# Kernel optimization log

Measured on AMD Instinct MI355X. Metric: run time of the kernel, lower is better.

Reference implementation:

```python
import jax, jax.numpy as jnp
import numpy as np

B, S, D, H = 2, 2048, 1024, 16
HD = D // H  # head dim = 64

def setup_inputs() -> dict:
    key = jax.random.key(0)
    k1, k2, k3, k4, k5 = jax.random.split(key, 5)
    return {
        "x": jax.random.normal(k1, (B, S, D), dtype=jnp.float32),
        "w_qkv": jax.random.normal(k2, (D, 3 * D), dtype=jnp.float32) * (1.0 / np.sqrt(D)),
        "b_qkv": jax.random.normal(k3, (3 * D,), dtype=jnp.float32) * 0.02,
        "w_out": jax.random.normal(k4, (D, D), dtype=jnp.float32) * (1.0 / np.sqrt(D)),
        "b_out": jax.random.normal(k5, (D,), dtype=jnp.float32) * 0.02,
        "c": 0,
    }

def reference(x, w_qkv, b_qkv, w_out, b_out, c):
    # fused QKV projection: [B,S,3D]
    qkv = jnp.einsum('bsd,de->bse', x, w_qkv) + b_qkv
    q, k, v = jnp.split(qkv, 3, axis=-1)
    # [B,S,D] -> [B,H,S,HD]
    split_heads = lambda t: t.reshape(B, S, H, HD).transpose(0, 2, 1, 3)
    q, k, v = split_heads(q), split_heads(k), split_heads(v)
    scale = 1.0 / np.sqrt(HD).astype(np.float32)
    scores = jnp.einsum('bhqd,bhkd->bhqk', q, k) * scale  # [B,H,S,S]
    probs = jax.nn.softmax(scores, axis=-1)
    # c==1 noise path references an undefined `const` in the original (dead/broken);
    # dropout probs are 0 -> identity (eval mode).
    attn = jnp.einsum('bhqk,bhkd->bhqd', probs, v)  # [B,H,S,HD]
    attn = attn.transpose(0, 2, 1, 3).reshape(B, S, D)
    out = jnp.einsum('bsd,de->bse', attn, w_out) + b_out
    return out
```

## Files before the change

### kernel.cpp

```cpp
#include <hip/hip_runtime.h>


typedef __attribute__((ext_vector_type(8))) short bs8;
typedef __attribute__((ext_vector_type(4))) short bs4;
typedef __attribute__((ext_vector_type(4))) float f32x4;

__device__ __forceinline__ f32x4 MFMA16K16(bs4 a, bs4 b, f32x4 c) {
#if defined(__HIP_DEVICE_COMPILE__)
  return __builtin_amdgcn_mfma_f32_16x16x16bf16_1k(a, b, c, 0, 0, 0);
#else
  return c;
#endif
}

#define QSCALE 0.18033688011112042f
#define MBOUND 24.0f

__device__ __forceinline__ unsigned short f2bf(float f) {
  union { float f; unsigned int u; } v; v.f = f;
  return (unsigned short)((v.u + 0x8000u) >> 16);
}

__device__ __forceinline__ unsigned int pkbf2(float a, float b) {
  union { float f; unsigned int u; } va, vb; va.f = a; vb.f = b;
#if defined(__HIP_DEVICE_COMPILE__)
  return __builtin_amdgcn_perm(vb.u + 0x8000u, va.u + 0x8000u, 0x07060302u);
#else
  return 0u;
#endif
}

__device__ __forceinline__ void async16(const unsigned short* g, unsigned short* lds) {
  __builtin_amdgcn_global_load_lds(
      (const __attribute__((address_space(1))) unsigned int*)g,
      (__attribute__((address_space(3))) unsigned int*)lds, 16, 0, 0);
}

__device__ __forceinline__ void stage_rows64(unsigned short* lds, const unsigned short* src,
                                             int ldk, int w, int l) {
#pragma unroll
  for (int i = 0; i < 4; ++i) {
    int row = (w * 4 + i) * 8 + (l >> 3);
    int cg  = (l & 7) ^ (l >> 3);
    async16(src + (size_t)row * ldk + cg * 8, lds + (w * 4 + i) * 512);
  }
}

__device__ __forceinline__ void stage_vt(unsigned short* lds, const unsigned short* vtb,
                                         int keyofs, int w, int l) {
#pragma unroll
  for (int i = 0; i < 4; ++i) {
    int row = (w * 4 + i) * 4 + (l >> 4);
    int cg = (l & 15) ^ (row & 15);
    async16(vtb + (size_t)row * 2048 + keyofs + cg * 8, lds + (w * 4 + i) * 512);
  }
}

__global__ __launch_bounds__(256) void cast_bf16_kernel(const float* __restrict__ src,
                                                        unsigned short* __restrict__ dst, int n) {
  int i = (blockIdx.x * 256 + threadIdx.x) * 8;
  if (i >= n) return;
  float4 a = *(const float4*)(src + i);
  float4 b = *(const float4*)(src + i + 4);
  union { bs8 v; unsigned short u[8]; } o;
  o.u[0] = f2bf(a.x); o.u[1] = f2bf(a.y); o.u[2] = f2bf(a.z); o.u[3] = f2bf(a.w);
  o.u[4] = f2bf(b.x); o.u[5] = f2bf(b.y); o.u[6] = f2bf(b.z); o.u[7] = f2bf(b.w);
  *(bs8*)(dst + i) = o.v;
}

__global__ __launch_bounds__(256) void transpose_cast_kernel(const float* __restrict__ src,
                                                             unsigned short* __restrict__ dst,
                                                             int R, int C) {
  __shared__ unsigned short tile[64][73];
  int c0 = blockIdx.x * 64, r0 = blockIdx.y * 64;
  int t = threadIdx.x;
  int rl = t >> 2, cb = (t & 3) * 16;
  const float* p = src + (size_t)(r0 + rl) * C + c0 + cb;
#pragma unroll
  for (int j = 0; j < 16; j += 4) {
    float4 f = *(const float4*)(p + j);
    tile[rl][cb + j + 0] = f2bf(f.x);
    tile[rl][cb + j + 1] = f2bf(f.y);
    tile[rl][cb + j + 2] = f2bf(f.z);
    tile[rl][cb + j + 3] = f2bf(f.w);
  }
  __syncthreads();
  int cl = t >> 2, rb = (t & 3) * 16;
  unsigned short* q = dst + (size_t)(c0 + cl) * R + r0 + rb;
#pragma unroll
  for (int j = 0; j < 16; ++j) q[j] = tile[rb + j][cl];
}

__global__ __launch_bounds__(256) void transpose_v_kernel(const unsigned short* __restrict__ v,
                                                          unsigned short* __restrict__ vt) {
  __shared__ unsigned short tile[64][73];
  int s0 = blockIdx.x * 64, bh = blockIdx.y;
  int t = threadIdx.x;
  int sl = t >> 2, hb = (t & 3) * 16;
  const unsigned short* p = v + ((size_t)bh * 2048 + s0 + sl) * 64 + hb;
#pragma unroll
  for (int j = 0; j < 16; ++j) tile[sl][hb + j] = p[j];
  __syncthreads();
  int hl = t >> 2, sb = (t & 3) * 16;
  unsigned short* q = vt + ((size_t)bh * 64 + hl) * 2048 + s0 + sb;
#pragma unroll
  for (int j = 0; j < 16; ++j) q[j] = tile[sb + j][hl];
}

#define GEMM_CORE(A_, Bt_)                                                        \
  __shared__ unsigned short As[128 * 64];                                         \
  __shared__ unsigned short Bs[128 * 64];                                         \
  int t = threadIdx.x, w = t >> 6, l = t & 63;                                    \
  int wm = w >> 1, wn = w & 1;                                                    \
  int bm = blockIdx.y, bn = blockIdx.x;                                           \
  const unsigned short* Abase = (A_) + (size_t)bm * 128 * 1024;                   \
  const unsigned short* Bbase = (Bt_) + (size_t)bn * 128 * 1024;                  \
  f32x4 zero4 = {0.f, 0.f, 0.f, 0.f};                                             \
  f32x4 acc[4][4];                                                                \
  _Pragma("unroll") for (int i = 0; i < 4; ++i)                                   \
  _Pragma("unroll") for (int j = 0; j < 4; ++j) acc[i][j] = zero4;                \
  for (int kt = 0; kt < 16; ++kt) {                                               \
    stage_rows64(As, Abase + kt * 64, 1024, w, l);                                \
    stage_rows64(Bs, Bbase + kt * 64, 1024, w, l);                                \
    __syncthreads();                                                              \
    _Pragma("unroll") for (int ks = 0; ks < 2; ++ks) {                            \
      bs8 af[4], bf[4];                                                           \
      _Pragma("unroll") for (int mt = 0; mt < 4; ++mt) {                          \
        int row = wm * 64 + mt * 16 + (l & 15);                                   \
        int c = ks * 4 + (l >> 4);                                                \
        af[mt] = *(const bs8*)&As[row * 64 + ((c ^ (row & 7)) * 8)];              \
      }                                                                           \
      _Pragma("unroll") for (int nt = 0; nt < 4; ++nt) {                          \
        int row = wn * 64 + nt * 16 + (l & 15);                                   \
        int c = ks * 4 + (l >> 4);                                                \
        bf[nt] = *(const bs8*)&Bs[row * 64 + ((c ^ (row & 7)) * 8)];              \
      }                                                                           \
      _Pragma("unroll") for (int mt = 0; mt < 4; ++mt)                            \
      _Pragma("unroll") for (int nt = 0; nt < 4; ++nt)                            \
        acc[mt][nt] = __builtin_amdgcn_mfma_f32_16x16x32_bf16(af[mt], bf[nt],     \
                                                              acc[mt][nt], 0, 0, 0); \
    }                                                                             \
    __syncthreads();                                                              \
  }

__global__ __launch_bounds__(256) void gemm_qkv_kernel(const unsigned short* __restrict__ A,
                                                       const unsigned short* __restrict__ Bt,
                                                       const float* __restrict__ bias,
                                                       unsigned short* __restrict__ qo,
                                                       unsigned short* __restrict__ ko,
                                                       unsigned short* __restrict__ vo) {
  GEMM_CORE(A, Bt)
#pragma unroll
  for (int nt = 0; nt < 4; ++nt) {
    int ng = bn * 128 + wn * 64 + nt * 16 + (l & 15);
    float bb = bias[ng];
    int sect = ng >> 10;
    int f = ng & 1023, h = f >> 6, hd = f & 63;
    unsigned short* dst = (sect == 0) ? qo : (sect == 1) ? ko : vo;
    float sc = (sect == 0) ? QSCALE : 1.0f;
#pragma unroll
    for (int mt = 0; mt < 4; ++mt)
#pragma unroll
      for (int r = 0; r < 4; ++r) {
        int mg = bm * 128 + wm * 64 + mt * 16 + (l >> 4) * 4 + r;
        int b = mg >> 11, s = mg & 2047;
        float val = (acc[mt][nt][r] + bb) * sc;
        dst[((size_t)(b * 16 + h) * 2048 + s) * 64 + hd] = f2bf(val);
      }
  }
}

__global__ __launch_bounds__(256) void gemm_out_kernel(const unsigned short* __restrict__ A,
                                                       const unsigned short* __restrict__ Bt,
                                                       const float* __restrict__ bias,
                                                       float* __restrict__ out) {
  GEMM_CORE(A, Bt)
#pragma unroll
  for (int nt = 0; nt < 4; ++nt) {
    int ng = bn * 128 + wn * 64 + nt * 16 + (l & 15);
    float bb = bias[ng];
#pragma unroll
    for (int mt = 0; mt < 4; ++mt)
#pragma unroll
      for (int r = 0; r < 4; ++r) {
        int mg = bm * 128 + wm * 64 + mt * 16 + (l >> 4) * 4 + r;
        out[(size_t)mg * 1024 + ng] = acc[mt][nt][r] + bb;
      }
  }
}

__global__ __launch_bounds__(256, 2) void attn_kernel(const unsigned short* __restrict__ Q,
                                                      const unsigned short* __restrict__ K,
                                                      const unsigned short* __restrict__ Vt,
                                                      unsigned short* __restrict__ Aout) {
  __shared__ unsigned short Ks[2][128 * 64];
  __shared__ unsigned short Vts[2][64 * 128];
  int t = threadIdx.x, w = t >> 6, l = t & 63;
  int m16 = l & 15, q = l >> 4;
  int qt = blockIdx.x, bh = blockIdx.y;
  const unsigned short* qbase = Q + (size_t)bh * 2048 * 64 + (size_t)qt * 128 * 64;
  const unsigned short* kbase = K + (size_t)bh * 2048 * 64;
  const unsigned short* vtbase = Vt + (size_t)bh * 64 * 2048;

  bs8 qf[2][2];
#pragma unroll
  for (int mt = 0; mt < 2; ++mt)
#pragma unroll
    for (int ks = 0; ks < 2; ++ks)
      qf[mt][ks] = *(const bs8*)(qbase + (size_t)(w * 32 + mt * 16 + m16) * 64 + ks * 32 + q * 8);

  stage_rows64(&Ks[0][0], kbase, 64, w, l);
  stage_vt(&Vts[0][0], vtbase, 0, w, l);
  __syncthreads();

  f32x4 zero4 = {0.f, 0.f, 0.f, 0.f};
  f32x4 minit = {-MBOUND, -MBOUND, -MBOUND, -MBOUND};
  f32x4 o[2][4];
  float lst[2] = {0.f, 0.f};
#pragma unroll
  for (int mt = 0; mt < 2; ++mt)
#pragma unroll
    for (int nh = 0; nh < 4; ++nh) o[mt][nh] = zero4;

  for (int kt = 0; kt < 16; ++kt) {
    int buf = kt & 1;
    if (kt < 15) {
      stage_rows64(&Ks[buf ^ 1][0], kbase + (size_t)(kt + 1) * 128 * 64, 64, w, l);
      stage_vt(&Vts[buf ^ 1][0], vtbase, (kt + 1) * 128, w, l);
    }
    const unsigned short* Kb = &Ks[buf][0];
    const unsigned short* Vb = &Vts[buf][0];

    f32x4 sAcc[2][8];
#pragma unroll
    for (int mt = 0; mt < 2; ++mt)
#pragma unroll
      for (int nt = 0; nt < 8; ++nt) sAcc[mt][nt] = minit;
#pragma unroll
    for (int ks = 0; ks < 2; ++ks) {
      bs8 kf[8];
#pragma unroll
      for (int nt = 0; nt < 8; ++nt) {
        int row = nt * 16 + m16;
        int c = ks * 4 + q;
        kf[nt] = *(const bs8*)&Kb[row * 64 + ((c ^ (row & 7)) * 8)];
      }
#pragma unroll
      for (int nt = 0; nt < 8; ++nt)
#pragma unroll
        for (int mt = 0; mt < 2; ++mt)
          sAcc[mt][nt] = __builtin_amdgcn_mfma_f32_16x16x32_bf16(kf[nt], qf[mt][ks],
                                                                 sAcc[mt][nt], 0, 0, 0);
    }

#pragma unroll
    for (int mt = 0; mt < 2; ++mt) {
      float rs = 0.f;
#pragma unroll
      for (int nt = 0; nt < 8; ++nt)
#pragma unroll
        for (int r = 0; r < 4; ++r) {
          float p = __builtin_amdgcn_exp2f(sAcc[mt][nt][r]);
          sAcc[mt][nt][r] = p;
          rs += p;
        }
      lst[mt] += rs;
    }

#pragma unroll
    for (int nt = 0; nt < 8; ++nt) {
      bs4 vf[4];
#pragma unroll
      for (int nh = 0; nh < 4; ++nh) {
        int vrow = nh * 16 + m16;
        int k = nt * 16 + q * 4;
        int chunk = k >> 3, within = k & 7;
        vf[nh] = *(const bs4*)&Vb[vrow * 128 + ((chunk ^ (vrow & 15)) * 8) + within];
      }
#pragma unroll
      for (int mt = 0; mt < 2; ++mt) {
        union { bs4 v; unsigned int u[2]; } pf;
        pf.u[0] = pkbf2(sAcc[mt][nt][0], sAcc[mt][nt][1]);
        pf.u[1] = pkbf2(sAcc[mt][nt][2], sAcc[mt][nt][3]);
#pragma unroll
        for (int nh = 0; nh < 4; ++nh)
          o[mt][nh] = MFMA16K16(vf[nh], pf.v, o[mt][nh]);
      }
    }
    __syncthreads();
  }

  int b = bh >> 4, h = bh & 15;
#pragma unroll
  for (int mt = 0; mt < 2; ++mt) {
    float l0 = lst[mt];
    l0 += __shfl_xor(l0, 16);
    l0 += __shfl_xor(l0, 32);
    float inv = 1.0f / l0;
    int s = qt * 128 + w * 32 + mt * 16 + m16;
#pragma unroll
    for (int nh = 0; nh < 4; ++nh)
#pragma unroll
      for (int r = 0; r < 4; ++r) {
        int hd = nh * 16 + q * 4 + r;
        Aout[((size_t)(b * 2048 + s)) * 1024 + h * 64 + hd] = f2bf(o[mt][nh][r] * inv);
      }
  }
}

extern "C" void kernel_launch(void* const* d_in, const int* in_sizes, int n_in,
                              void* d_out, int out_size, void* d_ws, size_t ws_size,
                              hipStream_t stream) {
  const float* x     = (const float*)d_in[0];
  const float* w_qkv = (const float*)d_in[1];
  const float* b_qkv = (const float*)d_in[2];
  const float* w_out = (const float*)d_in[3];
  const float* b_out = (const float*)d_in[4];
  float* out = (float*)d_out;

  char* ws = (char*)d_ws;
  unsigned short* xb    = (unsigned short*)(ws);
  unsigned short* wt1   = (unsigned short*)(ws + (8u << 20));
  unsigned short* wt2   = (unsigned short*)(ws + (14u << 20));
  unsigned short* qb    = (unsigned short*)(ws + (16u << 20));
  unsigned short* kb    = (unsigned short*)(ws + (24u << 20));
  unsigned short* vb    = (unsigned short*)(ws + (32u << 20));
  unsigned short* vtb   = (unsigned short*)(ws + (40u << 20));
  unsigned short* attnb = (unsigned short*)(ws + (48u << 20));

  cast_bf16_kernel<<<2048, 256, 0, stream>>>(x, xb, 4194304);
  transpose_cast_kernel<<<dim3(48, 16), 256, 0, stream>>>(w_qkv, wt1, 1024, 3072);
  transpose_cast_kernel<<<dim3(16, 16), 256, 0, stream>>>(w_out, wt2, 1024, 1024);
  gemm_qkv_kernel<<<dim3(24, 32), 256, 0, stream>>>(xb, wt1, b_qkv, qb, kb, vb);
  transpose_v_kernel<<<dim3(32, 32), 256, 0, stream>>>(vb, vtb);
  attn_kernel<<<dim3(16, 32), 256, 0, stream>>>(qb, kb, vtb, attnb);
  gemm_out_kernel<<<dim3(8, 32), 256, 0, stream>>>(attnb, wt2, b_out, out);
}
```

Before: 209.0 us.

## Swizzle V-transpose layout to cut LDS bank conflicts; use 8 waves in out-projection GEMM

The V transpose kernel now writes each row with a 4-element swap inside 8-element groups for half of the head-dim rows. The attention kernel's V fragment reads apply the matching inverse swizzle, which is meant to reduce LDS bank conflicts on the bs4 reads. Separately, the output-projection GEMM runs 512 threads (8 waves) per 128x128 tile, each wave holding a 32x64 sub-tile, to raise occupancy and latency hiding. The cost is more barrier participants and a smaller MFMA tile per wave, and the V layout now depends on a cross-kernel swizzle contract that must stay consistent.

```diff
diff --git a/kernel.cpp b/kernel.cpp
--- a/kernel.cpp
+++ b/kernel.cpp
@@ -43,6 +43,16 @@
     int row = (w * 4 + i) * 8 + (l >> 3);
     int cg  = (l & 7) ^ (l >> 3);
     async16(src + (size_t)row * ldk + cg * 8, lds + (w * 4 + i) * 512);
+  }
+}
+
+__device__ __forceinline__ void stage_rows64_8w(unsigned short* lds, const unsigned short* src,
+                                                int ldk, int w, int l) {
+#pragma unroll
+  for (int i = 0; i < 2; ++i) {
+    int row = (w * 2 + i) * 8 + (l >> 3);
+    int cg  = (l & 7) ^ (l >> 3);
+    async16(src + (size_t)row * ldk + cg * 8, lds + (w * 2 + i) * 512);
   }
 }
 
@@ -103,8 +113,9 @@
   __syncthreads();
   int hl = t >> 2, sb = (t & 3) * 16;
   unsigned short* q = vt + ((size_t)bh * 64 + hl) * 2048 + s0 + sb;
-#pragma unroll
-  for (int j = 0; j < 16; ++j) q[j] = tile[sb + j][hl];
+  int sw = (hl & 8) ? 4 : 0;
+#pragma unroll
+  for (int j = 0; j < 16; ++j) q[j ^ sw] = tile[sb + j][hl];
 }
 
 #define GEMM_CORE(A_, Bt_)                                                        \
@@ -170,20 +181,60 @@
   }
 }
 
-__global__ __launch_bounds__(256) void gemm_out_kernel(const unsigned short* __restrict__ A,
+__global__ __launch_bounds__(512) void gemm_out_kernel(const unsigned short* __restrict__ A,
                                                        const unsigned short* __restrict__ Bt,
                                                        const float* __restrict__ bias,
                                                        float* __restrict__ out) {
-  GEMM_CORE(A, Bt)
+  __shared__ unsigned short As[128 * 64];
+  __shared__ unsigned short Bs[128 * 64];
+  int t = threadIdx.x, w = t >> 6, l = t & 63;
+  int wm = w >> 1, wn = w & 1;
+  int bm = blockIdx.y, bn = blockIdx.x;
+  const unsigned short* Abase = A + (size_t)bm * 128 * 1024;
+  const unsigned short* Bbase = Bt + (size_t)bn * 128 * 1024;
+  f32x4 zero4 = {0.f, 0.f, 0.f, 0.f};
+  f32x4 acc[2][4];
+#pragma unroll
+  for (int i = 0; i < 2; ++i)
+#pragma unroll
+    for (int j = 0; j < 4; ++j) acc[i][j] = zero4;
+  for (int kt = 0; kt < 16; ++kt) {
+    stage_rows64_8w(As, Abase + kt * 64, 1024, w, l);
+    stage_rows64_8w(Bs, Bbase + kt * 64, 1024, w, l);
+    __syncthreads();
+#pragma unroll
+    for (int ks = 0; ks < 2; ++ks) {
+      bs8 af[2], bf[4];
+#pragma unroll
+      for (int mt = 0; mt < 2; ++mt) {
+        int row = wm * 32 + mt * 16 + (l & 15);
+        int c = ks * 4 + (l >> 4);
+        af[mt] = *(const bs8*)&As[row * 64 + ((c ^ (row & 7)) * 8)];
+      }
+#pragma unroll
+      for (int nt = 0; nt < 4; ++nt) {
+        int row = wn * 64 + nt * 16 + (l & 15);
+        int c = ks * 4 + (l >> 4);
+        bf[nt] = *(const bs8*)&Bs[row * 64 + ((c ^ (row & 7)) * 8)];
+      }
+#pragma unroll
+      for (int mt = 0; mt < 2; ++mt)
+#pragma unroll
+        for (int nt = 0; nt < 4; ++nt)
+          acc[mt][nt] = __builtin_amdgcn_mfma_f32_16x16x32_bf16(af[mt], bf[nt],
+                                                                acc[mt][nt], 0, 0, 0);
+    }
+    __syncthreads();
+  }
 #pragma unroll
   for (int nt = 0; nt < 4; ++nt) {
     int ng = bn * 128 + wn * 64 + nt * 16 + (l & 15);
     float bb = bias[ng];
 #pragma unroll
-    for (int mt = 0; mt < 4; ++mt)
+    for (int mt = 0; mt < 2; ++mt)
 #pragma unroll
       for (int r = 0; r < 4; ++r) {
-        int mg = bm * 128 + wm * 64 + mt * 16 + (l >> 4) * 4 + r;
+        int mg = bm * 128 + wm * 32 + mt * 16 + (l >> 4) * 4 + r;
         out[(size_t)mg * 1024 + ng] = acc[mt][nt][r] + bb;
       }
   }
@@ -213,14 +264,16 @@
   stage_vt(&Vts[0][0], vtbase, 0, w, l);
   __syncthreads();
 
+  f32x4 minit = {-MBOUND, -MBOUND, -MBOUND, -MBOUND};
   f32x4 zero4 = {0.f, 0.f, 0.f, 0.f};
-  f32x4 minit = {-MBOUND, -MBOUND, -MBOUND, -MBOUND};
   f32x4 o[2][4];
   float lst[2] = {0.f, 0.f};
 #pragma unroll
   for (int mt = 0; mt < 2; ++mt)
 #pragma unroll
     for (int nh = 0; nh < 4; ++nh) o[mt][nh] = zero4;
+
+  int vsw = (m16 >> 3) & 1;
 
   for (int kt = 0; kt < 16; ++kt) {
     int buf = kt & 1;
@@ -273,8 +326,8 @@
 #pragma unroll
       for (int nh = 0; nh < 4; ++nh) {
         int vrow = nh * 16 + m16;
-        int k = nt * 16 + q * 4;
-        int chunk = k >> 3, within = k & 7;
+        int chunk = nt * 2 + (q >> 1);
+        int within = ((q & 1) ^ vsw) * 4;
         vf[nh] = *(const bs4*)&Vb[vrow * 128 + ((chunk ^ (vrow & 15)) * 8) + within];
       }
 #pragma unroll
@@ -334,5 +387,5 @@
   gemm_qkv_kernel<<<dim3(24, 32), 256, 0, stream>>>(xb, wt1, b_qkv, qb, kb, vb);
   transpose_v_kernel<<<dim3(32, 32), 256, 0, stream>>>(vb, vtb);
   attn_kernel<<<dim3(16, 32), 256, 0, stream>>>(qb, kb, vtb, attnb);
-  gemm_out_kernel<<<dim3(8, 32), 256, 0, stream>>>(attnb, wt2, b_out, out);
-}
+  gemm_out_kernel<<<dim3(8, 32), 512, 0, stream>>>(attnb, wt2, b_out, out);
+}
```

New measurement: 206.4 us. No clear change (-1.3%).
